# Kernel optimization log

Hardware: AMD Instinct MI355X
Metric: run time of the kernel (lower is better)

Reference implementation:

```python
import jax, jax.numpy as jnp
import numpy as np

NUM_SEQ, NUM_RES = 512, 768
MSA_C, PAIR_C, NUM_HEAD = 64, 128, 8
VALUE_DIM = MSA_C // NUM_HEAD
EPS = 1e-5


def _layernorm(x, scale, bias):
    mu = jnp.mean(x, axis=-1, keepdims=True)
    var = jnp.var(x, axis=-1, keepdims=True)
    return (x - mu) * jax.lax.rsqrt(var + EPS) * scale + bias


def setup_inputs() -> dict:
    key = jax.random.key(0)
    ks = jax.random.split(key, 8)
    act = jax.random.normal(ks[0], (NUM_SEQ, NUM_RES, MSA_C), dtype=jnp.float32)
    mask = jnp.ones((NUM_SEQ, NUM_RES), dtype=jnp.float32)
    pair_act = jax.random.normal(ks[1], (NUM_RES, NUM_RES, PAIR_C), dtype=jnp.float32)
    # learned params
    act_scale = jnp.ones((MSA_C,), jnp.float32)
    act_bias = jnp.zeros((MSA_C,), jnp.float32)
    pair_scale = jnp.ones((PAIR_C,), jnp.float32)
    pair_bias = jnp.zeros((PAIR_C,), jnp.float32)
    w_pair_logits = jax.random.normal(ks[2], (NUM_HEAD, PAIR_C), jnp.float32) * (PAIR_C ** -0.5)
    v_proj = jax.random.normal(ks[3], (MSA_C, NUM_HEAD, VALUE_DIM), jnp.float32) * (MSA_C ** -0.5)
    w_gate = jax.random.normal(ks[4], (MSA_C, MSA_C), jnp.float32) * (MSA_C ** -0.5)
    w_out = jax.random.normal(ks[5], (MSA_C, MSA_C), jnp.float32) * (MSA_C ** -0.5)
    return {
        "act": act, "mask": mask, "pair_act": pair_act,
        "act_scale": act_scale, "act_bias": act_bias,
        "pair_scale": pair_scale, "pair_bias": pair_bias,
        "w_pair_logits": w_pair_logits, "v_proj": v_proj,
        "w_gate": w_gate, "w_out": w_out,
    }


def reference(act, mask, pair_act, act_scale, act_bias, pair_scale, pair_bias,
              w_pair_logits, v_proj, w_gate, w_out):
    act = _layernorm(act, act_scale, act_bias)            # [b, k, i]
    pair = _layernorm(pair_act, pair_scale, pair_bias)    # [q, k, c]
    logits = jnp.einsum('qkc,hc->hqk', pair, w_pair_logits)  # [h, q, k]
    # mask reduced over MSA rows; torch casts to bf16 before the bias add
    mask_max = jnp.max(mask, axis=0).astype(jnp.bfloat16)    # [k]
    logits = logits + 1e9 * (mask_max.astype(logits.dtype) - 1.0)
    weights = jax.nn.softmax(logits, axis=-1)                # [h, q, k]
    v = jnp.einsum('bki,ihc->bkhc', act, v_proj)             # [b, k, h, c]
    v_avg = jnp.einsum('hqk,bkhc->bqhc', weights, v)         # [b, q, h, c]
    v_avg = v_avg.reshape(v_avg.shape[0], v_avg.shape[1], -1)  # [b, q, h*c]
    gate = jax.nn.sigmoid(act @ w_gate.T)
    return (v_avg * gate) @ w_out.T
```

## Files before the change

### kernel.cpp

```cpp
#include <hip/hip_runtime.h>
#include <hip/hip_bf16.h>

#define NSEQ 512
#define NRES 768
#define MSAC 64
#define PAIRC 128
#define NHEAD 8

typedef __attribute__((ext_vector_type(8))) short short8_t;
typedef __attribute__((ext_vector_type(4))) float f32x4;

__device__ __forceinline__ float bf2f(unsigned short u){
  return __uint_as_float(((unsigned int)u) << 16);
}
__device__ __forceinline__ unsigned short f2bf(float f){
  unsigned int x = __float_as_uint(f);
  x += 0x7fffu + ((x >> 16) & 1u);
  return (unsigned short)(x >> 16);
}
__device__ __forceinline__ void glds16(const void* g, void* l){
  __builtin_amdgcn_global_load_lds(
      (const __attribute__((address_space(1))) unsigned int*)g,
      (__attribute__((address_space(3))) unsigned int*)l, 16, 0, 0);
}

__global__ __launch_bounds__(256) void k_prep2(
    const float* __restrict__ mask, const float* __restrict__ vproj,
    const float* __restrict__ wgate, const float* __restrict__ wout,
    const float* __restrict__ pscale, const float* __restrict__ pbias,
    const float* __restrict__ wl,
    float* __restrict__ bias, unsigned short* __restrict__ WvT,
    unsigned short* __restrict__ WgT, unsigned short* __restrict__ WoH,
    unsigned short* __restrict__ WoL, unsigned short* __restrict__ WST,
    float* __restrict__ AB)
{
  const int bid = blockIdx.x, tid = threadIdx.x;
  if (bid < 12){
    __shared__ float red[4][64];
    const int kk = bid*64 + (tid & 63);
    const int bs = tid >> 6;
    float m = -1e30f;
    for (int b = bs; b < NSEQ; b += 4) m = fmaxf(m, mask[(size_t)b*NRES + kk]);
    red[bs][tid & 63] = m;
    __syncthreads();
    if (tid < 64){
      float mm = fmaxf(fmaxf(red[0][tid], red[1][tid]),
                       fmaxf(red[2][tid], red[3][tid]));
      bias[bid*64 + tid] = 1e9f * (bf2f(f2bf(mm)) - 1.0f);
    }
  } else if (bid < 28){
    const int t = (bid - 12)*256 + tid;
    const int j = t >> 6, i = t & 63;
    WvT[t] = f2bf(vproj[i*64 + j]);
    WgT[t] = f2bf(wgate[t]);
    float wv = wout[t];
    unsigned short hh = f2bf(wv);
    WoH[t] = hh;
    WoL[t] = f2bf(wv - bf2f(hh));
  } else {
    #pragma unroll
    for (int i = 0; i < 4; ++i){
      int t = i*256 + tid;
      int h = t >> 7, c = t & 127;
      float w = pscale[c] * wl[h*PAIRC + c];
      unsigned short hh = f2bf(w);
      WST[h*PAIRC + c] = hh;
      WST[(h + 8)*PAIRC + c] = f2bf(w - bf2f(hh));
    }
    const int h = tid >> 5, cc = tid & 31;
    float pa = 0.f, pb = 0.f;
    for (int c = cc; c < PAIRC; c += 32){
      float w = wl[h*PAIRC + c];
      pa += pscale[c]*w;  pb += pbias[c]*w;
    }
    #pragma unroll
    for (int m = 1; m < 32; m <<= 1){
      pa += __shfl_xor(pa, m, 64);
      pb += __shfl_xor(pb, m, 64);
    }
    if (cc == 0){ AB[h] = pa; AB[8 + h] = pb; }
  }
}

__global__ __launch_bounds__(256) void k_pairact(
    const float* __restrict__ pair, const unsigned short* __restrict__ WST,
    const float* __restrict__ AB, const float* __restrict__ mbias,
    unsigned short* __restrict__ weights,
    const float* __restrict__ act, const float* __restrict__ ascale,
    const float* __restrict__ abias, const unsigned short* __restrict__ WvT,
    const unsigned short* __restrict__ WgT, unsigned short* __restrict__ v,
    unsigned short* __restrict__ gate)
{
  __shared__ __align__(16) unsigned char sm[24576];
  const int bid = blockIdx.x;
  const int tid = threadIdx.x;

  if (bid < 768){
    float (*lg)[NRES] = (float (*)[NRES])sm;
    const int q = bid;
    const int wv = tid >> 6, lane = tid & 63;
    const int lr = lane & 15, lcq = lane >> 4;

    short8_t wfrag[4];
    #pragma unroll
    for (int s = 0; s < 4; ++s)
      wfrag[s] = *(const short8_t*)(WST + lr*PAIRC + lcq*8 + s*32);

    const int hb = (lcq & 1) * 4;
    float A4[4], B4[4];
    #pragma unroll
    for (int r = 0; r < 4; ++r){ A4[r] = AB[hb + r]; B4[r] = AB[8 + hb + r]; }

    for (int tile = wv; tile < 48; tile += 4){
      const int k0 = tile * 16;
      const float* base = pair + ((size_t)q*NRES + k0 + lr)*PAIRC + lcq*8;
      f32x4 a1 = 0.f, a2 = 0.f;
      float s = 0.f, ss = 0.f;
      #pragma unroll
      for (int st = 0; st < 4; ++st){
        float4 u0 = *(const float4*)(base + st*32);
        float4 u1 = *(const float4*)(base + st*32 + 4);
        float xv[8] = {u0.x,u0.y,u0.z,u0.w,u1.x,u1.y,u1.z,u1.w};
        short8_t xh, xl;
        #pragma unroll
        for (int e = 0; e < 8; ++e){
          s += xv[e]; ss += xv[e]*xv[e];
          unsigned short hi = f2bf(xv[e]);
          xh[e] = (short)hi;
          xl[e] = (short)f2bf(xv[e] - bf2f(hi));
        }
        a1 = __builtin_amdgcn_mfma_f32_16x16x32_bf16(wfrag[st], xh, a1, 0, 0, 0);
        a2 = __builtin_amdgcn_mfma_f32_16x16x32_bf16(wfrag[st], xl, a2, 0, 0, 0);
      }
      s  += __shfl_xor(s, 16, 64);  ss += __shfl_xor(ss, 16, 64);
      s  += __shfl_xor(s, 32, 64);  ss += __shfl_xor(ss, 32, 64);
      const float mu  = s * (1.f/128.f);
      const float var = ss * (1.f/128.f) - mu*mu;
      const float rsq = rsqrtf(var + 1e-5f);
      float d[4];
      #pragma unroll
      for (int r = 0; r < 4; ++r)
        d[r] = a1[r] + __shfl_xor(a1[r], 32, 64) + a2[r];
      if (lane < 32){
        const int k = k0 + lr;
        #pragma unroll
        for (int r = 0; r < 4; ++r)
          lg[hb + r][k] = rsq * (d[r] - mu * A4[r]) + B4[r];
      }
    }
    __syncthreads();
    #pragma unroll
    for (int hh = 0; hh < 2; ++hh){
      int h = wv + hh*4;
      float mx = -1e30f;
      for (int kk = lane; kk < NRES; kk += 64) mx = fmaxf(mx, lg[h][kk] + mbias[kk]);
      #pragma unroll
      for (int m = 1; m < 64; m <<= 1) mx = fmaxf(mx, __shfl_xor(mx, m, 64));
      float sum = 0.f;
      for (int kk = lane; kk < NRES; kk += 64){
        float e = __expf(lg[h][kk] + mbias[kk] - mx);
        lg[h][kk] = e; sum += e;
      }
      #pragma unroll
      for (int m = 1; m < 64; m <<= 1) sum += __shfl_xor(sum, m, 64);
      float inv = 1.0f / sum;
      unsigned short* wrow = weights + ((size_t)h * NRES + q) * NRES;
      for (int kk = lane; kk < NRES; kk += 64) wrow[kk] = f2bf(lg[h][kk] * inv);
    }
  } else {
    unsigned short (*vt)[72] = (unsigned short (*)[72])sm;
    unsigned short (*gt)[72] = (unsigned short (*)[72])(sm + 9216);
    const int abid = bid - 768;
    const int b  = abid / 12;
    const int k0 = (abid % 12) * 64;
    const int w = tid >> 6, lane = tid & 63;
    const int lr = lane & 15;
    const int lc = lane >> 4;
    const int row = k0 + w*16 + lr;

    const float* arow = act + ((size_t)b*NRES + row)*MSAC;
    float x[2][8];
    #pragma unroll
    for (int s = 0; s < 2; ++s){
      float4 t0 = *(const float4*)(arow + s*32 + lc*8);
      float4 t1 = *(const float4*)(arow + s*32 + lc*8 + 4);
      x[s][0]=t0.x; x[s][1]=t0.y; x[s][2]=t0.z; x[s][3]=t0.w;
      x[s][4]=t1.x; x[s][5]=t1.y; x[s][6]=t1.z; x[s][7]=t1.w;
    }
    float ps = 0.f, pss = 0.f;
    #pragma unroll
    for (int s = 0; s < 2; ++s)
      #pragma unroll
      for (int e = 0; e < 8; ++e){ ps += x[s][e]; pss += x[s][e]*x[s][e]; }
    ps  += __shfl_xor(ps, 16, 64);  pss += __shfl_xor(pss, 16, 64);
    ps  += __shfl_xor(ps, 32, 64);  pss += __shfl_xor(pss, 32, 64);
    const float mu  = ps * (1.f/64.f);
    const float var = pss * (1.f/64.f) - mu*mu;
    const float rs  = rsqrtf(var + 1e-5f);

    short8_t a[2];
    #pragma unroll
    for (int s = 0; s < 2; ++s){
      float4 s0 = *(const float4*)(ascale + s*32 + lc*8);
      float4 s1 = *(const float4*)(ascale + s*32 + lc*8 + 4);
      float4 b0 = *(const float4*)(abias  + s*32 + lc*8);
      float4 b1 = *(const float4*)(abias  + s*32 + lc*8 + 4);
      const float sc[8] = {s0.x,s0.y,s0.z,s0.w,s1.x,s1.y,s1.z,s1.w};
      const float bs[8] = {b0.x,b0.y,b0.z,b0.w,b1.x,b1.y,b1.z,b1.w};
      #pragma unroll
      for (int e = 0; e < 8; ++e)
        a[s][e] = (short)f2bf((x[s][e] - mu)*rs*sc[e] + bs[e]);
    }

    short8_t bv[4][2], bg[4][2];
    #pragma unroll
    for (int mf = 0; mf < 4; ++mf){
      #pragma unroll
      for (int s = 0; s < 2; ++s){
        bv[mf][s] = *(const short8_t*)(WvT + (mf*16 + lr)*64 + s*32 + lc*8);
        bg[mf][s] = *(const short8_t*)(WgT + (mf*16 + lr)*64 + s*32 + lc*8);
      }
    }

    f32x4 accv[4], accg[4];
    #pragma unroll
    for (int mf = 0; mf < 4; ++mf){ accv[mf] = 0.f; accg[mf] = 0.f; }
    #pragma unroll
    for (int mf = 0; mf < 4; ++mf){
      #pragma unroll
      for (int s = 0; s < 2; ++s){
        accv[mf] = __builtin_amdgcn_mfma_f32_16x16x32_bf16(a[s], bv[mf][s], accv[mf], 0, 0, 0);
        accg[mf] = __builtin_amdgcn_mfma_f32_16x16x32_bf16(bg[mf][s], a[s], accg[mf], 0, 0, 0);
      }
    }

    #pragma unroll
    for (int mf = 0; mf < 4; ++mf){
      ushort4 ov;
      ov.x = f2bf(accv[mf][0]); ov.y = f2bf(accv[mf][1]);
      ov.z = f2bf(accv[mf][2]); ov.w = f2bf(accv[mf][3]);
      *(ushort4*)&vt[mf*16 + lr][w*16 + lc*4] = ov;
      ushort4 og;
      og.x = f2bf(1.0f/(1.0f + __expf(-accg[mf][0])));
      og.y = f2bf(1.0f/(1.0f + __expf(-accg[mf][1])));
      og.z = f2bf(1.0f/(1.0f + __expf(-accg[mf][2])));
      og.w = f2bf(1.0f/(1.0f + __expf(-accg[mf][3])));
      *(ushort4*)&gt[w*16 + lr][mf*16 + lc*4] = og;
    }
    __syncthreads();
    #pragma unroll
    for (int it = 0; it < 2; ++it){
      int fl = it*256 + tid;
      int j = fl >> 3, chunk = fl & 7;
      uint4 val = *(const uint4*)&vt[j][chunk*8];
      *(uint4*)(v + ((size_t)(j >> 3)*4096 + (size_t)b*8 + (j & 7))*NRES + k0 + chunk*8) = val;
    }
    #pragma unroll
    for (int it = 0; it < 2; ++it){
      int fl = it*256 + tid;
      int k = fl >> 3, chunk = fl & 7;
      uint4 val = *(const uint4*)&gt[k][chunk*8];
      *(uint4*)(gate + ((size_t)b*NRES + k0 + k)*MSAC + chunk*8) = val;
    }
  }
}

__global__ __launch_bounds__(256) void k_wavg(
    const unsigned short* __restrict__ V, const unsigned short* __restrict__ W,
    unsigned short* __restrict__ Y)
{
  __shared__ unsigned char smem[32768];

  const int flat = blockIdx.x;
  const int nid  = (flat & 7) * 192 + (flat >> 3);
  const int m    = nid % 192;
  const int by   = m % 6;
  const int bx   = m / 6;
  const int h    = nid / 192;

  const int tid = threadIdx.x, wid = tid >> 6, lane = tid & 63;
  const int wm = wid & 1, wn = wid >> 1;
  const unsigned short* Ag = V + (size_t)h*4096*768 + (size_t)bx*128*768;
  const unsigned short* Bg = W + (size_t)h*768*768 + (size_t)by*128*768;

  f32x4 acc[4][4];
  #pragma unroll
  for (int i=0;i<4;++i){
    #pragma unroll
    for (int jj=0;jj<4;++jj) acc[i][jj] = 0.f;
  }

  #define STAGE_K(bufsel, kt) { \
    unsigned char* Ab = smem + (bufsel)*16384; \
    unsigned char* Bb = Ab + 8192; \
    _Pragma("unroll") \
    for (int r = 0; r < 2; ++r){ \
      int cid = tid + r*256; \
      int rw = cid >> 2, ch = cid & 3; \
      int sc = ch ^ ((rw >> 1) & 3); \
      glds16(Ag + (size_t)rw*768 + (kt)*32 + sc*8, Ab + cid*16 - lane*16); \
      glds16(Bg + (size_t)rw*768 + (kt)*32 + sc*8, Bb + cid*16 - lane*16); \
    } }

  STAGE_K(0, 0);
  __syncthreads();
  const int c0 = lane >> 4;
  for (int kt = 0; kt < 24; ++kt){
    if (kt < 23) STAGE_K((kt+1)&1, kt+1);
    unsigned char* Ab = smem + (kt&1)*16384;
    unsigned char* Bb = Ab + 8192;
    short8_t af[4], bf[4];
    #pragma unroll
    for (int mf = 0; mf < 4; ++mf){
      int row = wm*64 + mf*16 + (lane & 15);
      int off = row*64 + ((c0 ^ ((row>>1)&3)) << 4);
      af[mf] = *(const short8_t*)(Ab + off);
    }
    #pragma unroll
    for (int nf = 0; nf < 4; ++nf){
      int row = wn*64 + nf*16 + (lane & 15);
      int off = row*64 + ((c0 ^ ((row>>1)&3)) << 4);
      bf[nf] = *(const short8_t*)(Bb + off);
    }
    #pragma unroll
    for (int mf = 0; mf < 4; ++mf){
      #pragma unroll
      for (int nf = 0; nf < 4; ++nf)
        acc[mf][nf] = __builtin_amdgcn_mfma_f32_16x16x32_bf16(af[mf], bf[nf], acc[mf][nf], 0, 0, 0);
    }
    __syncthreads();
  }
  #undef STAGE_K

  unsigned char* Ds = smem;
  #pragma unroll
  for (int mf = 0; mf < 4; ++mf){
    int bc = wm*64 + mf*16 + ((lane >> 4) << 2);
    #pragma unroll
    for (int nf = 0; nf < 4; ++nf){
      int q = wn*64 + nf*16 + (lane & 15);
      f32x4 a = acc[mf][nf];
      ushort4 o;
      o.x = f2bf(a[0]); o.y = f2bf(a[1]); o.z = f2bf(a[2]); o.w = f2bf(a[3]);
      int off = q*256 + bc*2; off ^= (q & 7) << 4;
      *(ushort4*)(Ds + off) = o;
    }
  }
  __syncthreads();
  unsigned short* Yb = Y + ((size_t)(h*32 + bx)*768 + by*128)*128;
  #pragma unroll
  for (int it = 0; it < 8; ++it){
    int fl = it*256 + tid;
    int q = fl >> 4, chunk = fl & 15;
    int off = q*256 + chunk*16; off ^= (q & 7) << 4;
    uint4 val = *(const uint4*)(Ds + off);
    *(uint4*)(Yb + (size_t)fl*8) = val;
  }
}

__global__ __launch_bounds__(256) void k_final(
    const unsigned short* __restrict__ Y, const unsigned short* __restrict__ gate,
    const unsigned short* __restrict__ WoH, const unsigned short* __restrict__ WoL,
    float* __restrict__ out)
{
  const int p = blockIdx.x;
  const int r = p & 7, t = p >> 3;
  const int b  = r*64 + (t & 63);
  const int q0 = (t >> 6) * 64;
  const int tid = threadIdx.x, w = tid >> 6, lane = tid & 63;
  const int lr = lane & 15, lc = lane >> 4;

  short8_t bh[4][2], bl[4][2];
  #pragma unroll
  for (int nf = 0; nf < 4; ++nf){
    #pragma unroll
    for (int s = 0; s < 2; ++s){
      bh[nf][s] = *(const short8_t*)(WoH + (nf*16 + lr)*64 + s*32 + lc*8);
      bl[nf][s] = *(const short8_t*)(WoL + (nf*16 + lr)*64 + s*32 + lc*8);
    }
  }

  const int q = q0 + w*16 + lr;
  short8_t ah[2], al[2];
  #pragma unroll
  for (int s = 0; s < 2; ++s){
    const int hh = s*4 + lc;
    short8_t y8 = *(const short8_t*)(Y + ((size_t)(hh*32 + (b >> 4))*768 + q)*128 + (b & 15)*8);
    short8_t g8 = *(const short8_t*)(gate + ((size_t)b*NRES + q)*MSAC + s*32 + lc*8);
    #pragma unroll
    for (int e = 0; e < 8; ++e){
      float pp = bf2f((unsigned short)y8[e]) * bf2f((unsigned short)g8[e]);
      unsigned short hi = f2bf(pp);
      ah[s][e] = (short)hi;
      al[s][e] = (short)f2bf(pp - bf2f(hi));
    }
  }

  f32x4 acc[4];
  #pragma unroll
  for (int nf = 0; nf < 4; ++nf) acc[nf] = 0.f;
  #pragma unroll
  for (int nf = 0; nf < 4; ++nf){
    #pragma unroll
    for (int s = 0; s < 2; ++s){
      acc[nf] = __builtin_amdgcn_mfma_f32_16x16x32_bf16(ah[s], bh[nf][s], acc[nf], 0, 0, 0);
      acc[nf] = __builtin_amdgcn_mfma_f32_16x16x32_bf16(al[s], bh[nf][s], acc[nf], 0, 0, 0);
      acc[nf] = __builtin_amdgcn_mfma_f32_16x16x32_bf16(ah[s], bl[nf][s], acc[nf], 0, 0, 0);
    }
  }

  #pragma unroll
  for (int nf = 0; nf < 4; ++nf){
    #pragma unroll
    for (int e = 0; e < 4; ++e){
      int qq = q0 + w*16 + lc*4 + e;
      out[((size_t)b*NRES + qq)*MSAC + nf*16 + lr] = acc[nf][e];
    }
  }
}

extern "C" void kernel_launch(void* const* d_in, const int* in_sizes, int n_in,
                              void* d_out, int out_size, void* d_ws, size_t ws_size,
                              hipStream_t stream) {
  (void)in_sizes; (void)n_in; (void)out_size; (void)ws_size;
  const float* act    = (const float*)d_in[0];
  const float* mask   = (const float*)d_in[1];
  const float* pair   = (const float*)d_in[2];
  const float* ascale = (const float*)d_in[3];
  const float* abias  = (const float*)d_in[4];
  const float* pscale = (const float*)d_in[5];
  const float* pbias  = (const float*)d_in[6];
  const float* wl     = (const float*)d_in[7];
  const float* vproj  = (const float*)d_in[8];
  const float* wgate  = (const float*)d_in[9];
  const float* wout   = (const float*)d_in[10];
  float* out = (float*)d_out;

  char* ws = (char*)d_ws;
  float*          mbias   = (float*)(ws);
  unsigned short* WvT     = (unsigned short*)(ws + 4096);
  unsigned short* WgT     = (unsigned short*)(ws + 12288);
  unsigned short* WoH     = (unsigned short*)(ws + 20480);
  unsigned short* WoL     = (unsigned short*)(ws + 28672);
  unsigned short* WST     = (unsigned short*)(ws + 36864);
  float*          AB      = (float*)(ws + 40960);
  unsigned short* weights = (unsigned short*)(ws + 45056);
  unsigned short* v       = (unsigned short*)(ws + 45056 + 9437184);
  unsigned short* gate    = (unsigned short*)(ws + 45056 + 9437184 + 50331648);
  unsigned short* y       = (unsigned short*)(ws + 45056 + 9437184 + 2*50331648ull);

  k_prep2<<<dim3(29), dim3(256), 0, stream>>>(mask, vproj, wgate, wout,
                                              pscale, pbias, wl,
                                              mbias, WvT, WgT, WoH, WoL, WST, AB);
  k_pairact<<<dim3(6912), dim3(256), 0, stream>>>(pair, WST, AB, mbias, weights,
                                                  act, ascale, abias, WvT, WgT, v, gate);
  k_wavg<<<dim3(1536), dim3(256), 0, stream>>>(v, weights, y);
  k_final<<<dim3(6144), dim3(256), 0, stream>>>(y, gate, WoH, WoL, out);
}
```

Before: 307.7 us.

## Software-pipeline pair tile loads and make act blocks loop over all residues

The pair-logits path now double-buffers global loads of the next 16-row tile in registers while the current tile is converted and run through MFMA. The act/gate path switches from one block per (batch, 64-residue chunk) to one block per batch row that loops over all 12 chunks, also double-buffering act loads and reusing the weight fragments it loaded once. The grid shrinks from 6912 to 1280 blocks. This aims to hide load latency and cut per-block setup, but it raises register pressure and reduces the block count available for load balancing.

```diff
diff --git a/kernel.cpp b/kernel.cpp
--- a/kernel.cpp
+++ b/kernel.cpp
@@ -111,43 +111,60 @@
     #pragma unroll
     for (int r = 0; r < 4; ++r){ A4[r] = AB[hb + r]; B4[r] = AB[8 + hb + r]; }
 
-    for (int tile = wv; tile < 48; tile += 4){
-      const int k0 = tile * 16;
-      const float* base = pair + ((size_t)q*NRES + k0 + lr)*PAIRC + lcq*8;
-      f32x4 a1 = 0.f, a2 = 0.f;
-      float s = 0.f, ss = 0.f;
-      #pragma unroll
-      for (int st = 0; st < 4; ++st){
-        float4 u0 = *(const float4*)(base + st*32);
-        float4 u1 = *(const float4*)(base + st*32 + 4);
-        float xv[8] = {u0.x,u0.y,u0.z,u0.w,u1.x,u1.y,u1.z,u1.w};
-        short8_t xh, xl;
-        #pragma unroll
-        for (int e = 0; e < 8; ++e){
-          s += xv[e]; ss += xv[e]*xv[e];
-          unsigned short hi = f2bf(xv[e]);
-          xh[e] = (short)hi;
-          xl[e] = (short)f2bf(xv[e] - bf2f(hi));
-        }
-        a1 = __builtin_amdgcn_mfma_f32_16x16x32_bf16(wfrag[st], xh, a1, 0, 0, 0);
-        a2 = __builtin_amdgcn_mfma_f32_16x16x32_bf16(wfrag[st], xl, a2, 0, 0, 0);
-      }
-      s  += __shfl_xor(s, 16, 64);  ss += __shfl_xor(ss, 16, 64);
-      s  += __shfl_xor(s, 32, 64);  ss += __shfl_xor(ss, 32, 64);
-      const float mu  = s * (1.f/128.f);
-      const float var = ss * (1.f/128.f) - mu*mu;
-      const float rsq = rsqrtf(var + 1e-5f);
-      float d[4];
-      #pragma unroll
-      for (int r = 0; r < 4; ++r)
-        d[r] = a1[r] + __shfl_xor(a1[r], 32, 64) + a2[r];
-      if (lane < 32){
-        const int k = k0 + lr;
-        #pragma unroll
-        for (int r = 0; r < 4; ++r)
-          lg[hb + r][k] = rsq * (d[r] - mu * A4[r]) + B4[r];
-      }
-    }
+#define LOADT(ub, tile_) { \
+    const float* base_ = pair + ((size_t)q*NRES + (tile_)*16 + lr)*PAIRC + lcq*8; \
+    _Pragma("unroll") \
+    for (int st = 0; st < 4; ++st){ \
+      ub[2*st]   = *(const float4*)(base_ + st*32); \
+      ub[2*st+1] = *(const float4*)(base_ + st*32 + 4); \
+    } }
+
+#define PROCT(ub, tile_) { \
+    f32x4 a1 = 0.f, a2 = 0.f; \
+    float s_ = 0.f, ss_ = 0.f; \
+    _Pragma("unroll") \
+    for (int st = 0; st < 4; ++st){ \
+      float xv[8] = {ub[2*st].x,ub[2*st].y,ub[2*st].z,ub[2*st].w, \
+                     ub[2*st+1].x,ub[2*st+1].y,ub[2*st+1].z,ub[2*st+1].w}; \
+      short8_t xh, xl; \
+      _Pragma("unroll") \
+      for (int e = 0; e < 8; ++e){ \
+        s_ += xv[e]; ss_ += xv[e]*xv[e]; \
+        unsigned short hi_ = f2bf(xv[e]); \
+        xh[e] = (short)hi_; \
+        xl[e] = (short)f2bf(xv[e] - bf2f(hi_)); \
+      } \
+      a1 = __builtin_amdgcn_mfma_f32_16x16x32_bf16(wfrag[st], xh, a1, 0, 0, 0); \
+      a2 = __builtin_amdgcn_mfma_f32_16x16x32_bf16(wfrag[st], xl, a2, 0, 0, 0); \
+    } \
+    s_  += __shfl_xor(s_, 16, 64);  ss_ += __shfl_xor(ss_, 16, 64); \
+    s_  += __shfl_xor(s_, 32, 64);  ss_ += __shfl_xor(ss_, 32, 64); \
+    const float mu_  = s_ * (1.f/128.f); \
+    const float var_ = ss_ * (1.f/128.f) - mu_*mu_; \
+    const float rsq_ = rsqrtf(var_ + 1e-5f); \
+    float d_[4]; \
+    _Pragma("unroll") \
+    for (int r = 0; r < 4; ++r) \
+      d_[r] = a1[r] + __shfl_xor(a1[r], 32, 64) + a2[r]; \
+    if (lane < 32){ \
+      const int k_ = (tile_)*16 + lr; \
+      _Pragma("unroll") \
+      for (int r = 0; r < 4; ++r) \
+        lg[hb + r][k_] = rsq_ * (d_[r] - mu_ * A4[r]) + B4[r]; \
+    } }
+
+    float4 uA[8], uB[8];
+    LOADT(uA, wv);
+    #pragma unroll
+    for (int it = 0; it < 6; ++it){
+      const int t = wv + it*8;
+      LOADT(uB, t+4);
+      PROCT(uA, t);
+      if (it < 5) LOADT(uA, t+8);
+      PROCT(uB, t+4);
+    }
+#undef LOADT
+#undef PROCT
     __syncthreads();
     #pragma unroll
     for (int hh = 0; hh < 2; ++hh){
@@ -170,47 +187,10 @@
   } else {
     unsigned short (*vt)[72] = (unsigned short (*)[72])sm;
     unsigned short (*gt)[72] = (unsigned short (*)[72])(sm + 9216);
-    const int abid = bid - 768;
-    const int b  = abid / 12;
-    const int k0 = (abid % 12) * 64;
+    const int b  = bid - 768;
     const int w = tid >> 6, lane = tid & 63;
     const int lr = lane & 15;
     const int lc = lane >> 4;
-    const int row = k0 + w*16 + lr;
-
-    const float* arow = act + ((size_t)b*NRES + row)*MSAC;
-    float x[2][8];
-    #pragma unroll
-    for (int s = 0; s < 2; ++s){
-      float4 t0 = *(const float4*)(arow + s*32 + lc*8);
-      float4 t1 = *(const float4*)(arow + s*32 + lc*8 + 4);
-      x[s][0]=t0.x; x[s][1]=t0.y; x[s][2]=t0.z; x[s][3]=t0.w;
-      x[s][4]=t1.x; x[s][5]=t1.y; x[s][6]=t1.z; x[s][7]=t1.w;
-    }
-    float ps = 0.f, pss = 0.f;
-    #pragma unroll
-    for (int s = 0; s < 2; ++s)
-      #pragma unroll
-      for (int e = 0; e < 8; ++e){ ps += x[s][e]; pss += x[s][e]*x[s][e]; }
-    ps  += __shfl_xor(ps, 16, 64);  pss += __shfl_xor(pss, 16, 64);
-    ps  += __shfl_xor(ps, 32, 64);  pss += __shfl_xor(pss, 32, 64);
-    const float mu  = ps * (1.f/64.f);
-    const float var = pss * (1.f/64.f) - mu*mu;
-    const float rs  = rsqrtf(var + 1e-5f);
-
-    short8_t a[2];
-    #pragma unroll
-    for (int s = 0; s < 2; ++s){
-      float4 s0 = *(const float4*)(ascale + s*32 + lc*8);
-      float4 s1 = *(const float4*)(ascale + s*32 + lc*8 + 4);
-      float4 b0 = *(const float4*)(abias  + s*32 + lc*8);
-      float4 b1 = *(const float4*)(abias  + s*32 + lc*8 + 4);
-      const float sc[8] = {s0.x,s0.y,s0.z,s0.w,s1.x,s1.y,s1.z,s1.w};
-      const float bs[8] = {b0.x,b0.y,b0.z,b0.w,b1.x,b1.y,b1.z,b1.w};
-      #pragma unroll
-      for (int e = 0; e < 8; ++e)
-        a[s][e] = (short)f2bf((x[s][e] - mu)*rs*sc[e] + bs[e]);
-    }
 
     short8_t bv[4][2], bg[4][2];
     #pragma unroll
@@ -222,46 +202,92 @@
       }
     }
 
-    f32x4 accv[4], accg[4];
-    #pragma unroll
-    for (int mf = 0; mf < 4; ++mf){ accv[mf] = 0.f; accg[mf] = 0.f; }
-    #pragma unroll
-    for (int mf = 0; mf < 4; ++mf){
-      #pragma unroll
-      for (int s = 0; s < 2; ++s){
-        accv[mf] = __builtin_amdgcn_mfma_f32_16x16x32_bf16(a[s], bv[mf][s], accv[mf], 0, 0, 0);
-        accg[mf] = __builtin_amdgcn_mfma_f32_16x16x32_bf16(bg[mf][s], a[s], accg[mf], 0, 0, 0);
-      }
-    }
-
-    #pragma unroll
-    for (int mf = 0; mf < 4; ++mf){
-      ushort4 ov;
-      ov.x = f2bf(accv[mf][0]); ov.y = f2bf(accv[mf][1]);
-      ov.z = f2bf(accv[mf][2]); ov.w = f2bf(accv[mf][3]);
-      *(ushort4*)&vt[mf*16 + lr][w*16 + lc*4] = ov;
-      ushort4 og;
-      og.x = f2bf(1.0f/(1.0f + __expf(-accg[mf][0])));
-      og.y = f2bf(1.0f/(1.0f + __expf(-accg[mf][1])));
-      og.z = f2bf(1.0f/(1.0f + __expf(-accg[mf][2])));
-      og.w = f2bf(1.0f/(1.0f + __expf(-accg[mf][3])));
-      *(ushort4*)&gt[w*16 + lr][mf*16 + lc*4] = og;
-    }
-    __syncthreads();
-    #pragma unroll
-    for (int it = 0; it < 2; ++it){
-      int fl = it*256 + tid;
-      int j = fl >> 3, chunk = fl & 7;
-      uint4 val = *(const uint4*)&vt[j][chunk*8];
-      *(uint4*)(v + ((size_t)(j >> 3)*4096 + (size_t)b*8 + (j & 7))*NRES + k0 + chunk*8) = val;
-    }
-    #pragma unroll
-    for (int it = 0; it < 2; ++it){
-      int fl = it*256 + tid;
-      int k = fl >> 3, chunk = fl & 7;
-      uint4 val = *(const uint4*)&gt[k][chunk*8];
-      *(uint4*)(gate + ((size_t)b*NRES + k0 + k)*MSAC + chunk*8) = val;
-    }
+#define LOADX(xb, k0v) { \
+    const float* arow_ = act + ((size_t)b*NRES + (k0v) + w*16 + lr)*MSAC; \
+    _Pragma("unroll") \
+    for (int s = 0; s < 2; ++s){ \
+      float4 t0 = *(const float4*)(arow_ + s*32 + lc*8); \
+      float4 t1 = *(const float4*)(arow_ + s*32 + lc*8 + 4); \
+      xb[s][0]=t0.x; xb[s][1]=t0.y; xb[s][2]=t0.z; xb[s][3]=t0.w; \
+      xb[s][4]=t1.x; xb[s][5]=t1.y; xb[s][6]=t1.z; xb[s][7]=t1.w; \
+    } }
+
+#define PROCA(xb, k0v) { \
+    float ps = 0.f, pss = 0.f; \
+    _Pragma("unroll") \
+    for (int s = 0; s < 2; ++s) \
+      _Pragma("unroll") \
+      for (int e = 0; e < 8; ++e){ ps += xb[s][e]; pss += xb[s][e]*xb[s][e]; } \
+    ps  += __shfl_xor(ps, 16, 64);  pss += __shfl_xor(pss, 16, 64); \
+    ps  += __shfl_xor(ps, 32, 64);  pss += __shfl_xor(pss, 32, 64); \
+    const float mu_ = ps*(1.f/64.f); \
+    const float var_ = pss*(1.f/64.f) - mu_*mu_; \
+    const float rs_ = rsqrtf(var_ + 1e-5f); \
+    short8_t a_[2]; \
+    _Pragma("unroll") \
+    for (int s = 0; s < 2; ++s){ \
+      float4 s0 = *(const float4*)(ascale + s*32 + lc*8); \
+      float4 s1 = *(const float4*)(ascale + s*32 + lc*8 + 4); \
+      float4 b0 = *(const float4*)(abias  + s*32 + lc*8); \
+      float4 b1 = *(const float4*)(abias  + s*32 + lc*8 + 4); \
+      const float sc_[8] = {s0.x,s0.y,s0.z,s0.w,s1.x,s1.y,s1.z,s1.w}; \
+      const float bs_[8] = {b0.x,b0.y,b0.z,b0.w,b1.x,b1.y,b1.z,b1.w}; \
+      _Pragma("unroll") \
+      for (int e = 0; e < 8; ++e) \
+        a_[s][e] = (short)f2bf((xb[s][e] - mu_)*rs_*sc_[e] + bs_[e]); \
+    } \
+    f32x4 accv[4], accg[4]; \
+    _Pragma("unroll") \
+    for (int mf = 0; mf < 4; ++mf){ accv[mf] = 0.f; accg[mf] = 0.f; } \
+    _Pragma("unroll") \
+    for (int mf = 0; mf < 4; ++mf){ \
+      _Pragma("unroll") \
+      for (int s = 0; s < 2; ++s){ \
+        accv[mf] = __builtin_amdgcn_mfma_f32_16x16x32_bf16(a_[s], bv[mf][s], accv[mf], 0, 0, 0); \
+        accg[mf] = __builtin_amdgcn_mfma_f32_16x16x32_bf16(bg[mf][s], a_[s], accg[mf], 0, 0, 0); \
+      } \
+    } \
+    _Pragma("unroll") \
+    for (int mf = 0; mf < 4; ++mf){ \
+      ushort4 ov; \
+      ov.x = f2bf(accv[mf][0]); ov.y = f2bf(accv[mf][1]); \
+      ov.z = f2bf(accv[mf][2]); ov.w = f2bf(accv[mf][3]); \
+      *(ushort4*)&vt[mf*16 + lr][w*16 + lc*4] = ov; \
+      ushort4 og; \
+      og.x = f2bf(1.0f/(1.0f + __expf(-accg[mf][0]))); \
+      og.y = f2bf(1.0f/(1.0f + __expf(-accg[mf][1]))); \
+      og.z = f2bf(1.0f/(1.0f + __expf(-accg[mf][2]))); \
+      og.w = f2bf(1.0f/(1.0f + __expf(-accg[mf][3]))); \
+      *(ushort4*)&gt[w*16 + lr][mf*16 + lc*4] = og; \
+    } \
+    __syncthreads(); \
+    _Pragma("unroll") \
+    for (int it2 = 0; it2 < 2; ++it2){ \
+      int fl = it2*256 + tid; \
+      int j_ = fl >> 3, chunk_ = fl & 7; \
+      uint4 val = *(const uint4*)&vt[j_][chunk_*8]; \
+      *(uint4*)(v + ((size_t)(j_ >> 3)*4096 + (size_t)b*8 + (j_ & 7))*NRES + (k0v) + chunk_*8) = val; \
+    } \
+    _Pragma("unroll") \
+    for (int it2 = 0; it2 < 2; ++it2){ \
+      int fl = it2*256 + tid; \
+      int k_ = fl >> 3, chunk_ = fl & 7; \
+      uint4 val = *(const uint4*)&gt[k_][chunk_*8]; \
+      *(uint4*)(gate + ((size_t)b*NRES + (k0v) + k_)*MSAC + chunk_*8) = val; \
+    } \
+    __syncthreads(); }
+
+    float xA[2][8], xB[2][8];
+    LOADX(xA, 0);
+    #pragma unroll
+    for (int c = 0; c < 12; c += 2){
+      LOADX(xB, (c+1)*64);
+      PROCA(xA, c*64);
+      if (c + 2 < 12) LOADX(xA, (c+2)*64);
+      PROCA(xB, (c+1)*64);
+    }
+#undef LOADX
+#undef PROCA
   }
 }
 
@@ -452,7 +478,7 @@
   k_prep2<<<dim3(29), dim3(256), 0, stream>>>(mask, vproj, wgate, wout,
                                               pscale, pbias, wl,
                                               mbias, WvT, WgT, WoH, WoL, WST, AB);
-  k_pairact<<<dim3(6912), dim3(256), 0, stream>>>(pair, WST, AB, mbias, weights,
+  k_pairact<<<dim3(1280), dim3(256), 0, stream>>>(pair, WST, AB, mbias, weights,
                                                   act, ascale, abias, WvT, WgT, v, gate);
   k_wavg<<<dim3(1536), dim3(256), 0, stream>>>(v, weights, y);
   k_final<<<dim3(6144), dim3(256), 0, stream>>>(y, gate, WoH, WoL, out);
```

Measured after the change: 392.7 us. 27.7% more time.

## Split pair-logit blocks into quarters and move softmax to a separate kernel

Applied to the files above, without the earlier changes.

Each query row's pair-logit computation is now spread over four blocks instead of one, each handling 12 of the 48 key tiles. The fp32 logits go to a global workspace instead of shared memory. A new k_soft kernel then reads them back, applies the mask bias and softmax, and writes the bf16 weights. The aim is to fix load imbalance: the 768 heavy pair blocks were few and long compared with the act blocks. The cost is an extra kernel launch plus about 19MB of logits written and read back through global memory. It also reduces shared memory per block and hoists the weight-fragment loads in the act branch ahead of the LayerNorm.

```diff
diff --git a/kernel.cpp b/kernel.cpp
--- a/kernel.cpp
+++ b/kernel.cpp
@@ -84,20 +84,19 @@
 
 __global__ __launch_bounds__(256) void k_pairact(
     const float* __restrict__ pair, const unsigned short* __restrict__ WST,
-    const float* __restrict__ AB, const float* __restrict__ mbias,
-    unsigned short* __restrict__ weights,
+    const float* __restrict__ AB, float* __restrict__ logits,
     const float* __restrict__ act, const float* __restrict__ ascale,
     const float* __restrict__ abias, const unsigned short* __restrict__ WvT,
     const unsigned short* __restrict__ WgT, unsigned short* __restrict__ v,
     unsigned short* __restrict__ gate)
 {
-  __shared__ __align__(16) unsigned char sm[24576];
+  __shared__ __align__(16) unsigned char sm[18432];
   const int bid = blockIdx.x;
   const int tid = threadIdx.x;
 
-  if (bid < 768){
-    float (*lg)[NRES] = (float (*)[NRES])sm;
-    const int q = bid;
+  if (bid < 3072){
+    const int q = bid >> 2;
+    const int quarter = bid & 3;
     const int wv = tid >> 6, lane = tid & 63;
     const int lr = lane & 15, lcq = lane >> 4;
 
@@ -111,7 +110,9 @@
     #pragma unroll
     for (int r = 0; r < 4; ++r){ A4[r] = AB[hb + r]; B4[r] = AB[8 + hb + r]; }
 
-    for (int tile = wv; tile < 48; tile += 4){
+    #pragma unroll
+    for (int i = 0; i < 3; ++i){
+      const int tile = quarter*12 + wv + 4*i;
       const int k0 = tile * 16;
       const float* base = pair + ((size_t)q*NRES + k0 + lr)*PAIRC + lcq*8;
       f32x4 a1 = 0.f, a2 = 0.f;
@@ -145,38 +146,29 @@
         const int k = k0 + lr;
         #pragma unroll
         for (int r = 0; r < 4; ++r)
-          lg[hb + r][k] = rsq * (d[r] - mu * A4[r]) + B4[r];
+          logits[(size_t)q*6144 + (hb + r)*768 + k] = rsq * (d[r] - mu * A4[r]) + B4[r];
       }
-    }
-    __syncthreads();
-    #pragma unroll
-    for (int hh = 0; hh < 2; ++hh){
-      int h = wv + hh*4;
-      float mx = -1e30f;
-      for (int kk = lane; kk < NRES; kk += 64) mx = fmaxf(mx, lg[h][kk] + mbias[kk]);
-      #pragma unroll
-      for (int m = 1; m < 64; m <<= 1) mx = fmaxf(mx, __shfl_xor(mx, m, 64));
-      float sum = 0.f;
-      for (int kk = lane; kk < NRES; kk += 64){
-        float e = __expf(lg[h][kk] + mbias[kk] - mx);
-        lg[h][kk] = e; sum += e;
-      }
-      #pragma unroll
-      for (int m = 1; m < 64; m <<= 1) sum += __shfl_xor(sum, m, 64);
-      float inv = 1.0f / sum;
-      unsigned short* wrow = weights + ((size_t)h * NRES + q) * NRES;
-      for (int kk = lane; kk < NRES; kk += 64) wrow[kk] = f2bf(lg[h][kk] * inv);
     }
   } else {
     unsigned short (*vt)[72] = (unsigned short (*)[72])sm;
     unsigned short (*gt)[72] = (unsigned short (*)[72])(sm + 9216);
-    const int abid = bid - 768;
+    const int abid = bid - 3072;
     const int b  = abid / 12;
     const int k0 = (abid % 12) * 64;
     const int w = tid >> 6, lane = tid & 63;
     const int lr = lane & 15;
     const int lc = lane >> 4;
     const int row = k0 + w*16 + lr;
+
+    short8_t bv[4][2], bg[4][2];
+    #pragma unroll
+    for (int mf = 0; mf < 4; ++mf){
+      #pragma unroll
+      for (int s = 0; s < 2; ++s){
+        bv[mf][s] = *(const short8_t*)(WvT + (mf*16 + lr)*64 + s*32 + lc*8);
+        bg[mf][s] = *(const short8_t*)(WgT + (mf*16 + lr)*64 + s*32 + lc*8);
+      }
+    }
 
     const float* arow = act + ((size_t)b*NRES + row)*MSAC;
     float x[2][8];
@@ -210,16 +202,6 @@
       #pragma unroll
       for (int e = 0; e < 8; ++e)
         a[s][e] = (short)f2bf((x[s][e] - mu)*rs*sc[e] + bs[e]);
-    }
-
-    short8_t bv[4][2], bg[4][2];
-    #pragma unroll
-    for (int mf = 0; mf < 4; ++mf){
-      #pragma unroll
-      for (int s = 0; s < 2; ++s){
-        bv[mf][s] = *(const short8_t*)(WvT + (mf*16 + lr)*64 + s*32 + lc*8);
-        bg[mf][s] = *(const short8_t*)(WgT + (mf*16 + lr)*64 + s*32 + lc*8);
-      }
     }
 
     f32x4 accv[4], accg[4];
@@ -262,6 +244,40 @@
       uint4 val = *(const uint4*)&gt[k][chunk*8];
       *(uint4*)(gate + ((size_t)b*NRES + k0 + k)*MSAC + chunk*8) = val;
     }
+  }
+}
+
+__global__ __launch_bounds__(256) void k_soft(
+    const float* __restrict__ logits, const float* __restrict__ mbias,
+    unsigned short* __restrict__ weights)
+{
+  __shared__ float lgf[6144];
+  const int q = blockIdx.x, tid = threadIdx.x;
+  const float* src = logits + (size_t)q*6144;
+  #pragma unroll
+  for (int i = 0; i < 6; ++i){
+    int idx = (i*256 + tid)*4;
+    *(float4*)&lgf[idx] = *(const float4*)(src + idx);
+  }
+  __syncthreads();
+  const int wv = tid >> 6, lane = tid & 63;
+  #pragma unroll
+  for (int hh = 0; hh < 2; ++hh){
+    int h = wv + hh*4;
+    float mx = -1e30f;
+    for (int kk = lane; kk < NRES; kk += 64) mx = fmaxf(mx, lgf[h*768 + kk] + mbias[kk]);
+    #pragma unroll
+    for (int m = 1; m < 64; m <<= 1) mx = fmaxf(mx, __shfl_xor(mx, m, 64));
+    float sum = 0.f;
+    for (int kk = lane; kk < NRES; kk += 64){
+      float e = __expf(lgf[h*768 + kk] + mbias[kk] - mx);
+      lgf[h*768 + kk] = e; sum += e;
+    }
+    #pragma unroll
+    for (int m = 1; m < 64; m <<= 1) sum += __shfl_xor(sum, m, 64);
+    float inv = 1.0f / sum;
+    unsigned short* wrow = weights + ((size_t)h * NRES + q) * NRES;
+    for (int kk = lane; kk < NRES; kk += 64) wrow[kk] = f2bf(lgf[h*768 + kk] * inv);
   }
 }
 
@@ -448,12 +464,14 @@
   unsigned short* v       = (unsigned short*)(ws + 45056 + 9437184);
   unsigned short* gate    = (unsigned short*)(ws + 45056 + 9437184 + 50331648);
   unsigned short* y       = (unsigned short*)(ws + 45056 + 9437184 + 2*50331648ull);
+  float*          logits  = (float*)(ws + 45056 + 9437184 + 3*50331648ull);
 
   k_prep2<<<dim3(29), dim3(256), 0, stream>>>(mask, vproj, wgate, wout,
                                               pscale, pbias, wl,
                                               mbias, WvT, WgT, WoH, WoL, WST, AB);
-  k_pairact<<<dim3(6912), dim3(256), 0, stream>>>(pair, WST, AB, mbias, weights,
+  k_pairact<<<dim3(9216), dim3(256), 0, stream>>>(pair, WST, AB, logits,
                                                   act, ascale, abias, WvT, WgT, v, gate);
+  k_soft<<<dim3(768), dim3(256), 0, stream>>>(logits, mbias, weights);
   k_wavg<<<dim3(1536), dim3(256), 0, stream>>>(v, weights, y);
   k_final<<<dim3(6144), dim3(256), 0, stream>>>(y, gate, WoH, WoL, out);
 }
```

After: 313.2 us. No clear change (+1.8%).
